# Performance work log

Measured on AMD Instinct MI355X. Metric: run time of the kernel, lower is better.

The kernel has to match this reference:

```python
import jax, jax.numpy as jnp
import numpy as np


def _lin_interp(x, out_size):
    # x: [..., T_in]; matches torch F.interpolate(mode='linear', align_corners=False)
    t_in = x.shape[-1]
    scale = t_in / out_size
    pos = (jnp.arange(out_size, dtype=jnp.float32) + 0.5) * scale - 0.5
    pos = jnp.clip(pos, 0.0, t_in - 1)
    lo = jnp.floor(pos).astype(jnp.int32)
    hi = jnp.minimum(lo + 1, t_in - 1)
    w = (pos - lo.astype(jnp.float32)).astype(x.dtype)
    return x[..., lo] * (1.0 - w) + x[..., hi] * w


def _lin_init(k, fan_in, shape):
    lim = 1.0 / np.sqrt(fan_in)
    return jax.random.uniform(k, shape, jnp.float32, -lim, lim)


def setup_inputs() -> dict:
    key = jax.random.key(0)
    ks = jax.random.split(key, 32)
    B, T, NMEL = 8, 1024, 80
    TV, H, W = 32, 112, 112
    S = 4  # max_speakers
    d = {}
    d['audio_input'] = jax.random.normal(ks[0], (B, T, NMEL), jnp.float32)
    d['video_input'] = jax.random.normal(ks[1], (B, TV, 3, H, W), jnp.float32)
    d['w_ae'] = _lin_init(ks[2], 80, (80, 256)); d['b_ae'] = _lin_init(ks[3], 80, (256,))
    d['ln_g'] = jnp.ones((256,), jnp.float32); d['ln_b'] = jnp.zeros((256,), jnp.float32)
    d['w_a1'] = _lin_init(ks[4], 256, (256, 512)); d['b_a1'] = _lin_init(ks[5], 256, (512,))
    d['w_a2'] = _lin_init(ks[6], 512, (512, 256)); d['b_a2'] = _lin_init(ks[7], 512, (256,))
    fan = 3 * 7 * 7
    d['conv_w'] = _lin_init(ks[8], fan, (64, 3, 7, 7)); d['conv_b'] = _lin_init(ks[9], fan, (64,))
    d['w_vfc'] = _lin_init(ks[10], 64, (64, 256)); d['b_vfc'] = _lin_init(ks[11], 64, (256,))
    d['w_f1'] = _lin_init(ks[12], 512, (512, 512)); d['b_f1'] = _lin_init(ks[13], 512, (512,))
    d['w_f2'] = _lin_init(ks[14], 512, (512, 256)); d['b_f2'] = _lin_init(ks[15], 512, (256,))
    d['heads_w'] = _lin_init(ks[16], 256, (S, 256, 80)); d['heads_b'] = _lin_init(ks[17], 256, (S, 80))
    d['w_spk'] = _lin_init(ks[18], 256, (256, S)); d['b_spk'] = _lin_init(ks[19], 256, (S,))
    return d


def reference(audio_input, video_input, w_ae, b_ae, ln_g, ln_b, w_a1, b_a1, w_a2, b_a2,
              conv_w, conv_b, w_vfc, b_vfc, w_f1, b_f1, w_f2, b_f2,
              heads_w, heads_b, w_spk, b_spk):
    # ---- audio branch ----
    a = audio_input @ w_ae + b_ae                      # [B,T,256]
    mu = a.mean(-1, keepdims=True)
    var = a.var(-1, keepdims=True)
    a = (a - mu) * jax.lax.rsqrt(var + 1e-5) * ln_g + ln_b
    a = jax.nn.relu(a @ w_a1 + b_a1) @ w_a2 + b_a2     # dropout is identity at eval
    # ---- video branch ----
    B, TV, C, H, W = video_input.shape
    v = video_input.reshape(B * TV, C, H, W)
    v = jax.lax.conv_general_dilated(v, conv_w, (2, 2), [(3, 3), (3, 3)],
                                     dimension_numbers=('NCHW', 'OIHW', 'NCHW'))
    v = v + conv_b[None, :, None, None]
    v = v.mean((2, 3))                                  # AdaptiveAvgPool2d((1,1))
    v = (v @ w_vfc + b_vfc).reshape(B, TV, 256)
    T = a.shape[1]
    if TV != T:
        v = _lin_interp(v.transpose(0, 2, 1), T).transpose(0, 2, 1)  # [B,T,256]
    # ---- fusion ----
    f = jnp.concatenate([a, v], axis=-1)                # [B,T,512]
    f = jax.nn.relu(f @ w_f1 + b_f1) @ w_f2 + b_f2      # [B,T,256]
    # ---- per-speaker heads as one batched GEMM ----
    specs = jnp.einsum('btd,sdo->bsto', f, heads_w) + heads_b[None, :, None, :]  # [B,S,T,80]
    # ---- specs -> waveforms (vectorized over batch x speakers) ----
    S = specs.shape[1]
    wave_len = T * 160  # samples_per_frame = 160
    noise = jax.random.normal(jax.random.key(1234), (B, S, wave_len), jnp.float32) * 0.1
    energy = _lin_interp(specs.sum(-1), wave_len)       # [B,S,wave_len]
    waveforms = noise * (energy * 0.5 + 0.5)
    # ---- speaker classifier ----
    speaker_logits = f.mean(1) @ w_spk + b_spk          # [B,S]
    return waveforms, specs, speaker_logits
```

## Files before the change

kernel.cpp:

```cpp
#include <hip/hip_runtime.h>
#include <hip/hip_bf16.h>
#include <math.h>

typedef _Float16 f16;
typedef f16 f16x8 __attribute__((ext_vector_type(8)));
typedef f16 f16x4 __attribute__((ext_vector_type(4)));
typedef float f32x4 __attribute__((ext_vector_type(4)));

template<int MT, int RELU, int OUT, int XTRA = 0>
__global__ __launch_bounds__(256) void hgemm(
    const f16* __restrict__ A, const f16* __restrict__ Wt,
    const float* __restrict__ bias,
    void* __restrict__ Cout, int ldc, int col_off,
    int N, int K, float* __restrict__ colsum)
{
  static_assert(MT == 64 || MT == 128, "MT");
  constexpr int MI = MT / 32;
  if (XTRA) {
    if (blockIdx.y == 4) {
      const float* v256 = colsum;
      f16* fb = (f16*)Cout;
      const int base = blockIdx.x * 16384 + (int)threadIdx.x;
#pragma unroll 4
      for (int i = 0; i < 64; i++) {
        const int idx = base + i * 256;
        const int c = idx & 255;
        const int t = (idx >> 8) & 1023;
        const int b = idx >> 18;
        float pos = ((float)t + 0.5f) * 0.03125f - 0.5f;
        pos = fminf(fmaxf(pos, 0.0f), 31.0f);
        const int lo = (int)floorf(pos);
        int hi = lo + 1; if (hi > 31) hi = 31;
        const float w = pos - (float)lo;
        const float vl = v256[(size_t)(b * 32 + lo) * 256 + c];
        const float vh = v256[(size_t)(b * 32 + hi) * 256 + c];
        fb[(size_t)(b * 1024 + t) * 512 + 256 + c] = (f16)(vl * (1.0f - w) + vh * w);
      }
      return;
    }
  }
  __shared__ __align__(16) f16 As[2][MT * 64];
  __shared__ __align__(16) f16 Bs[2][64 * 64];
  const int tid = threadIdx.x;
  const int wave = tid >> 6, lane = tid & 63;
  const int wm = (wave >> 1) * (MT / 2);
  const int wn = (wave & 1) * 32;
  const int m0 = blockIdx.x * MT;
  const int n0 = blockIdx.y * 64;
  const int q = lane >> 4, r16 = lane & 15;

  const int rA0 = tid >> 3, gA0 = tid & 7;
  const f16* pA = A + (size_t)(m0 + rA0) * K + gA0 * 8;
  const f16* pB = Wt + (size_t)(n0 + rA0) * K + gA0 * 8;
  const int sbase = rA0 * 128 + ((gA0 ^ (rA0 & 7)) * 16);

  f32x4 acc[MI][2];
#pragma unroll
  for (int mi = 0; mi < MI; mi++)
#pragma unroll
    for (int ni = 0; ni < 2; ni++) acc[mi][ni] = (f32x4)0.f;

  f16x8 ar[MI], br[2];
#pragma unroll
  for (int j = 0; j < MI; j++) ar[j] = *(const f16x8*)(pA + (size_t)j * 32 * K);
#pragma unroll
  for (int j = 0; j < 2; j++) br[j] = *(const f16x8*)(pB + (size_t)j * 32 * K);

  const int iters = K >> 6;
  int p = 0;
  for (int it = 0; it < iters; it++) {
#pragma unroll
    for (int j = 0; j < MI; j++)
      *(f16x8*)((char*)As[p] + sbase + j * 4096) = ar[j];
#pragma unroll
    for (int j = 0; j < 2; j++)
      *(f16x8*)((char*)Bs[p] + sbase + j * 4096) = br[j];
    if (it + 1 < iters) {
      const int ko = (it + 1) << 6;
#pragma unroll
      for (int j = 0; j < MI; j++) ar[j] = *(const f16x8*)(pA + (size_t)j * 32 * K + ko);
#pragma unroll
      for (int j = 0; j < 2; j++) br[j] = *(const f16x8*)(pB + (size_t)j * 32 * K + ko);
    }
    __syncthreads();
#pragma unroll
    for (int h = 0; h < 2; h++) {
      const int kg = h * 4 + q;
      f16x8 af[MI], bf[2];
#pragma unroll
      for (int mi = 0; mi < MI; mi++) {
        const int row = wm + mi * 16 + r16;
        af[mi] = *(const f16x8*)((char*)As[p] + row * 128 + ((kg ^ (row & 7)) * 16));
      }
#pragma unroll
      for (int ni = 0; ni < 2; ni++) {
        const int row = wn + ni * 16 + r16;
        bf[ni] = *(const f16x8*)((char*)Bs[p] + row * 128 + ((kg ^ (row & 7)) * 16));
      }
#pragma unroll
      for (int mi = 0; mi < MI; mi++)
#pragma unroll
        for (int ni = 0; ni < 2; ni++)
          acc[mi][ni] = __builtin_amdgcn_mfma_f32_16x16x32_f16(
              af[mi], bf[ni], acc[mi][ni], 0, 0, 0);
    }
    p ^= 1;
  }

#pragma unroll
  for (int ni = 0; ni < 2; ni++) {
    const int n = n0 + wn + ni * 16 + r16;
    const float bv = bias[n];
    float csum = 0.f;
#pragma unroll
    for (int mi = 0; mi < MI; mi++) {
#pragma unroll
      for (int rr = 0; rr < 4; rr++) {
        const int m = m0 + wm + mi * 16 + q * 4 + rr;
        float v = acc[mi][ni][rr] + bv;
        if (RELU) v = fmaxf(v, 0.f);
        if (OUT == 2) csum += v;
        ((f16*)Cout)[(size_t)m * ldc + col_off + n] = (f16)v;
      }
    }
    if (OUT == 2) {
      csum += __shfl_xor(csum, 16);
      csum += __shfl_xor(csum, 32);
      if (q == 0) atomicAdd(&colsum[(m0 >> 10) * 256 + n], csum);
    }
  }
}

__global__ __launch_bounds__(256) void prep_video_kernel(
    const float* __restrict__ video, float* __restrict__ Sg,
    const float* __restrict__ w_ae, const float* __restrict__ w_a1,
    const float* __restrict__ w_a2, const float* __restrict__ w_f1,
    const float* __restrict__ w_f2, const float* __restrict__ heads_w,
    const float* __restrict__ heads_b,
    f16* __restrict__ wae_t, f16* __restrict__ wa1_t,
    f16* __restrict__ wa2_t, f16* __restrict__ wf1_t, f16* __restrict__ wf2_t,
    f16* __restrict__ wh_t, float* __restrict__ bp, float* __restrict__ colsum)
{
  if (blockIdx.x < 768) {
    const int img = blockIdx.x;
    const float* p = video + (size_t)img * 12544;
    __shared__ float rowS[2][112];
    __shared__ float c0s[112], c1s[112], c109s[112], c110s[112], c111s[112];
    __shared__ float base[14];
    __shared__ float sE[7], sO[7];
    const int t = threadIdx.x;
    if (t < 224) {
      const int r = t >> 1;
      const int par = t & 1;
      const float* rp = p + r * 112 + par;
      float s = 0.f;
#pragma unroll
      for (int i = 0; i < 56; i++) s += rp[2 * i];
      rowS[par][r] = s;
      if (par == 0) { c0s[r] = rp[0]; c110s[r] = rp[110]; }
      else { c1s[r] = rp[0]; c109s[r] = rp[108]; c111s[r] = rp[110]; }
    }
    __syncthreads();
    if (t < 14) {
      const int arr = t >> 1;
      const int rp = t & 1;
      const float* src = (arr == 0) ? rowS[0] : (arr == 1) ? rowS[1] :
                         (arr == 2) ? c0s : (arr == 3) ? c1s :
                         (arr == 4) ? c109s : (arr == 5) ? c110s : c111s;
      float s = 0.f;
      for (int r = rp; r < 112; r += 2) s += src[r];
      base[t] = s;
    }
    __syncthreads();
    if (t < 7) {
      float se, so;
      switch (t) {
        case 0: se = base[2] - base[8] - base[12]; so = base[3] - base[9] - base[13]; break;
        case 1: se = base[0] - base[10];           so = base[1] - base[11];           break;
        case 2: se = base[2] - base[12];           so = base[3] - base[13];           break;
        case 3: se = base[0];                      so = base[1];                      break;
        case 4: se = base[2];                      so = base[3];                      break;
        case 5: se = base[0] - base[4];            so = base[1] - base[5];            break;
        default: se = base[2] - base[6];           so = base[3] - base[7];            break;
      }
      sE[t] = se; sO[t] = so;
    }
    __syncthreads();
    if (t < 49) {
      const int kh = t / 7, kw = t % 7;
      auto ccol = [&](int r) -> float {
        switch (kw) {
          case 0: return rowS[1][r] - c109s[r] - c111s[r];
          case 1: return rowS[0][r] - c110s[r];
          case 2: return rowS[1][r] - c111s[r];
          case 3: return rowS[0][r];
          case 4: return rowS[1][r];
          case 5: return rowS[0][r] - c0s[r];
          default: return rowS[1][r] - c1s[r];
        }
      };
      float v;
      switch (kh) {
        case 0: v = sO[kw] - ccol(109) - ccol(111); break;
        case 1: v = sE[kw] - ccol(110);             break;
        case 2: v = sO[kw] - ccol(111);             break;
        case 3: v = sE[kw];                         break;
        case 4: v = sO[kw];                         break;
        case 5: v = sE[kw] - ccol(0);               break;
        default: v = sO[kw] - ccol(1);              break;
      }
      Sg[(size_t)img * 49 + t] = v;
    }
    return;
  }
  int idx = (blockIdx.x - 768) * 256 + threadIdx.x;
  if (idx < 32768) {
    const int n = idx >> 7, k = idx & 127;
    wae_t[idx] = (f16)(k < 80 ? w_ae[k * 256 + n] : 0.f);
    return;
  }
  idx -= 32768;
  if (idx < 131072) { const int n = idx >> 8, k = idx & 255; wa1_t[idx] = (f16)w_a1[k * 512 + n]; return; }
  idx -= 131072;
  if (idx < 131072) { const int n = idx >> 9, k = idx & 511; wa2_t[idx] = (f16)w_a2[k * 256 + n]; return; }
  idx -= 131072;
  if (idx < 262144) { const int n = idx >> 9, k = idx & 511; wf1_t[idx] = (f16)w_f1[k * 512 + n]; return; }
  idx -= 262144;
  if (idx < 131072) { const int n = idx >> 9, k = idx & 511; wf2_t[idx] = (f16)w_f2[k * 256 + n]; return; }
  idx -= 131072;
  if (idx < 81920) {
    const int n = idx >> 8, d = idx & 255;
    const int s = n / 80, o = n - s * 80;
    wh_t[idx] = (f16)heads_w[(size_t)(s * 256 + d) * 80 + o];
    return;
  }
  idx -= 81920;
  if (idx < 320) { bp[idx] = heads_b[idx]; return; }
  idx -= 320;
  if (idx < 2048) colsum[idx] = 0.f;
}

__global__ __launch_bounds__(256) void vpool_aeln_kernel(
    const float* __restrict__ Sg, const float* __restrict__ conv_w,
    const float* __restrict__ conv_b, const float* __restrict__ w_vfc,
    const float* __restrict__ b_vfc, float* __restrict__ v256,
    const float* __restrict__ audio, const f16* __restrict__ wae_t,
    const float* __restrict__ b_ae, const float* __restrict__ ln_g,
    const float* __restrict__ ln_b, f16* __restrict__ a1)
{
  __shared__ __align__(16) f16 As[64 * 128];
  __shared__ __align__(16) f16 Bs[256 * 128];
  const int tid = threadIdx.x;
  if (blockIdx.x < 256) {
    float* vp = (float*)As;
    const int n = blockIdx.x;
    if (tid < 64) {
      float acc = 0.f;
      const float* s = Sg + (size_t)n * 147;
#pragma unroll 7
      for (int k = 0; k < 147; k++) acc = fmaf(conv_w[tid * 147 + k], s[k], acc);
      vp[tid] = conv_b[tid] + acc * (1.0f / 3136.0f);
    }
    __syncthreads();
    float acc = 0.f;
#pragma unroll
    for (int k = 0; k < 64; k++) acc = fmaf(vp[k], w_vfc[k * 256 + tid], acc);
    v256[(size_t)n * 256 + tid] = acc + b_vfc[tid];
    return;
  }
  const int m0 = (blockIdx.x - 256) * 64;
  const int wave = tid >> 6, lane = tid & 63;
  const int q = lane >> 4, r16 = lane & 15;
#pragma unroll
  for (int c = tid; c < 1024; c += 256) {
    const int row = c >> 4, g = c & 15;
    f16x8 val = (f16x8)(f16)0.f;
    if (g < 10) {
      const float* src = audio + (size_t)(m0 + row) * 80 + g * 8;
      const float4 u = *(const float4*)src;
      const float4 w = *(const float4*)(src + 4);
      val[0] = (f16)u.x; val[1] = (f16)u.y; val[2] = (f16)u.z; val[3] = (f16)u.w;
      val[4] = (f16)w.x; val[5] = (f16)w.y; val[6] = (f16)w.z; val[7] = (f16)w.w;
    }
    *(f16x8*)((char*)As + row * 256 + ((g ^ (row & 7)) * 16)) = val;
  }
#pragma unroll
  for (int c = tid; c < 4096; c += 256) {
    const int row = c >> 4, g = c & 15;
    *(f16x8*)((char*)Bs + row * 256 + ((g ^ (row & 7)) * 16)) =
        *(const f16x8*)(wae_t + (size_t)row * 128 + g * 8);
  }
  __syncthreads();
  const int wm = wave * 16;
  f32x4 acc[16];
#pragma unroll
  for (int nf = 0; nf < 16; nf++) acc[nf] = (f32x4)0.f;
#pragma unroll
  for (int kf = 0; kf < 4; kf++) {
    const int kg = kf * 4 + q;
    const int ar = wm + r16;
    const f16x8 af = *(const f16x8*)((char*)As + ar * 256 + ((kg ^ (ar & 7)) * 16));
#pragma unroll
    for (int nf = 0; nf < 16; nf++) {
      const int br = nf * 16 + r16;
      const f16x8 bf = *(const f16x8*)((char*)Bs + br * 256 + ((kg ^ (br & 7)) * 16));
      acc[nf] = __builtin_amdgcn_mfma_f32_16x16x32_f16(af, bf, acc[nf], 0, 0, 0);
    }
  }
  float rs[4] = {0.f, 0.f, 0.f, 0.f};
  float rq[4] = {0.f, 0.f, 0.f, 0.f};
#pragma unroll
  for (int nf = 0; nf < 16; nf++) {
    const float bv = b_ae[nf * 16 + r16];
#pragma unroll
    for (int rr = 0; rr < 4; rr++) {
      const float v = acc[nf][rr] + bv;
      acc[nf][rr] = v;
      rs[rr] += v; rq[rr] += v * v;
    }
  }
#pragma unroll
  for (int off = 1; off < 16; off <<= 1) {
#pragma unroll
    for (int rr = 0; rr < 4; rr++) {
      rs[rr] += __shfl_xor(rs[rr], off);
      rq[rr] += __shfl_xor(rq[rr], off);
    }
  }
  float mu[4], ri[4];
#pragma unroll
  for (int rr = 0; rr < 4; rr++) {
    mu[rr] = rs[rr] * (1.0f / 256.0f);
    const float var = rq[rr] * (1.0f / 256.0f) - mu[rr] * mu[rr];
    ri[rr] = rsqrtf(var + 1e-5f);
  }
#pragma unroll
  for (int nf = 0; nf < 16; nf++) {
    const int col = nf * 16 + r16;
    const float g = ln_g[col], b = ln_b[col];
#pragma unroll
    for (int rr = 0; rr < 4; rr++) {
      const int row = m0 + wm + q * 4 + rr;
      a1[(size_t)row * 256 + col] = (f16)((acc[nf][rr] - mu[rr]) * ri[rr] * g + b);
    }
  }
}

__global__ __launch_bounds__(256) void heads_energy_kernel(
    const f16* __restrict__ A, const f16* __restrict__ Wt,
    const float* __restrict__ bias, float* __restrict__ specs,
    float* __restrict__ energy)
{
  __shared__ __align__(16) f16 As[64 * 256];
  __shared__ __align__(16) f16 Bs[80 * 256];
  const int tid = threadIdx.x;
  const int s = blockIdx.y;
  const int m0 = blockIdx.x * 64;
  const int wave = tid >> 6, lane = tid & 63;
  const int q = lane >> 4, r16 = lane & 15;
#pragma unroll
  for (int c = tid; c < 2048; c += 256) {
    const int row = c >> 5, g = c & 31;
    *(f16x8*)((char*)As + row * 512 + ((g ^ (row & 7)) * 16)) =
        *(const f16x8*)(A + (size_t)(m0 + row) * 256 + g * 8);
  }
#pragma unroll
  for (int c = tid; c < 2560; c += 256) {
    const int row = c >> 5, g = c & 31;
    *(f16x8*)((char*)Bs + row * 512 + ((g ^ (row & 7)) * 16)) =
        *(const f16x8*)(Wt + (size_t)(s * 80 + row) * 256 + g * 8);
  }
  __syncthreads();
  const int wm = wave * 16;
  f32x4 acc[5];
#pragma unroll
  for (int nf = 0; nf < 5; nf++) acc[nf] = (f32x4)0.f;
#pragma unroll
  for (int kf = 0; kf < 8; kf++) {
    const int kg = kf * 4 + q;
    const int ar = wm + r16;
    const f16x8 af = *(const f16x8*)((char*)As + ar * 512 + ((kg ^ (ar & 7)) * 16));
#pragma unroll
    for (int nf = 0; nf < 5; nf++) {
      const int br = nf * 16 + r16;
      const f16x8 bf = *(const f16x8*)((char*)Bs + br * 512 + ((kg ^ (br & 7)) * 16));
      acc[nf] = __builtin_amdgcn_mfma_f32_16x16x32_f16(af, bf, acc[nf], 0, 0, 0);
    }
  }
  float bv[5];
#pragma unroll
  for (int nf = 0; nf < 5; nf++) bv[nf] = bias[s * 80 + nf * 16 + r16];
  float rs[4] = {0.f, 0.f, 0.f, 0.f};
#pragma unroll
  for (int rr = 0; rr < 4; rr++) {
    const int row = m0 + wm + q * 4 + rr;
    const int b_ = row >> 10, t_ = row & 1023;
    float* dst = specs + ((size_t)((b_ * 4 + s) * 1024 + t_)) * 80;
#pragma unroll
    for (int nf = 0; nf < 5; nf++) {
      const float v = acc[nf][rr] + bv[nf];
      rs[rr] += v;
      dst[nf * 16 + r16] = v;
    }
  }
#pragma unroll
  for (int off = 1; off < 16; off <<= 1) {
#pragma unroll
    for (int rr = 0; rr < 4; rr++) rs[rr] += __shfl_xor(rs[rr], off);
  }
  if (r16 == 0) {
#pragma unroll
    for (int rr = 0; rr < 4; rr++) {
      const int row = m0 + wm + q * 4 + rr;
      const int b_ = row >> 10, t_ = row & 1023;
      energy[((b_ * 4 + s) << 10) + t_] = rs[rr];
    }
  }
}

__device__ __forceinline__ unsigned rotl32(unsigned x, int d) {
  return (x << d) | (x >> (32 - d));
}

__device__ __forceinline__ float erfinv_fast(float x) {
  const float t = (1.0f - x) * (1.0f + x);
  float w = -__logf(t);
  float p;
  if (w < 5.0f) {
    w = w - 2.5f;
    p = 2.81022636e-08f;
    p = fmaf(p, w, 3.43273939e-07f);
    p = fmaf(p, w, -3.5233877e-06f);
    p = fmaf(p, w, -4.39150654e-06f);
    p = fmaf(p, w, 0.00021858087f);
    p = fmaf(p, w, -0.00125372503f);
    p = fmaf(p, w, -0.00417768164f);
    p = fmaf(p, w, 0.246640727f);
    p = fmaf(p, w, 1.50140941f);
  } else {
    w = sqrtf(w) - 3.0f;
    p = -0.000200214257f;
    p = fmaf(p, w, 0.000100950558f);
    p = fmaf(p, w, 0.00134934322f);
    p = fmaf(p, w, -0.00367342844f);
    p = fmaf(p, w, 0.00573950773f);
    p = fmaf(p, w, -0.0076224613f);
    p = fmaf(p, w, 0.00943887047f);
    p = fmaf(p, w, 1.00167406f);
    p = fmaf(p, w, 2.83297682f);
  }
  return p * x;
}

__global__ __launch_bounds__(256) void waveform_kernel(
    const float* __restrict__ energy, float* __restrict__ out,
    const float* __restrict__ colsum, const float* __restrict__ w_spk,
    const float* __restrict__ b_spk, float* __restrict__ logits)
{
  if (blockIdx.x == 5120) {
    const int idx = threadIdx.x;
    if (idx < 32) {
      const int b = idx >> 2, s = idx & 3;
      const float* cs = colsum + b * 256;
      float acc = 0.f;
#pragma unroll 8
      for (int d = 0; d < 256; d++)
        acc = fmaf(cs[d] * (1.0f / 1024.0f), w_spk[d * 4 + s], acc);
      logits[b * 4 + s] = acc + b_spk[s];
    }
    return;
  }
  const unsigned base = (blockIdx.x * 256 + threadIdx.x) * 4;
  const unsigned ks0 = 0u, ks1 = 1234u;
  const unsigned ks2 = 0x1BD11BDAu ^ ks0 ^ ks1;
  unsigned x0[4], x1[4];
#pragma unroll
  for (int j = 0; j < 4; j++) { x0[j] = ks0; x1[j] = base + (unsigned)j + ks1; }
#define TFR(r)                                                     \
  _Pragma("unroll") for (int j = 0; j < 4; j++) {                  \
    x0[j] += x1[j]; x1[j] = rotl32(x1[j], r); x1[j] ^= x0[j];      \
  }
#define TFK(ka, kb)                                                \
  _Pragma("unroll") for (int j = 0; j < 4; j++) {                  \
    x0[j] += (ka); x1[j] += (kb);                                  \
  }
  TFR(13) TFR(15) TFR(26) TFR(6)  TFK(ks1, ks2 + 1u)
  TFR(17) TFR(29) TFR(16) TFR(24) TFK(ks2, ks0 + 2u)
  TFR(13) TFR(15) TFR(26) TFR(6)  TFK(ks0, ks1 + 3u)
  TFR(17) TFR(29) TFR(16) TFR(24) TFK(ks1, ks2 + 4u)
  TFR(13) TFR(15) TFR(26) TFR(6)  TFK(ks2, ks0 + 5u)
#undef TFR
#undef TFK
  const unsigned i0 = base % 163840u;
  const unsigned bs = base / 163840u;
  const float* e = energy + (size_t)bs * 1024;
  float4 o;
#pragma unroll
  for (int j = 0; j < 4; j++) {
    const unsigned bits = x0[j] ^ x1[j];
    const float f = __uint_as_float((bits >> 9) | 0x3f800000u) - 1.0f;
    const float minv = -0.99999994f;
    const float u = fmaxf(minv, fmaf(f, 2.0f, minv));
    const float noise = 1.41421354f * erfinv_fast(u) * 0.1f;
    float pos = ((float)(i0 + j) + 0.5f) * 0.00625f - 0.5f;
    pos = fminf(fmaxf(pos, 0.0f), 1023.0f);
    const int lo = (int)floorf(pos);
    int hi = lo + 1; if (hi > 1023) hi = 1023;
    const float w = pos - (float)lo;
    const float ev = e[lo] * (1.0f - w) + e[hi] * w;
    ((float*)&o)[j] = noise * fmaf(ev, 0.5f, 0.5f);
  }
  *(float4*)(out + base) = o;
}

extern "C" void kernel_launch(void* const* d_in, const int* in_sizes, int n_in,
                              void* d_out, int out_size, void* d_ws, size_t ws_size,
                              hipStream_t stream)
{
  (void)in_sizes; (void)n_in; (void)out_size; (void)ws_size;
  const float* audio   = (const float*)d_in[0];
  const float* video   = (const float*)d_in[1];
  const float* w_ae    = (const float*)d_in[2];
  const float* b_ae    = (const float*)d_in[3];
  const float* ln_g    = (const float*)d_in[4];
  const float* ln_b    = (const float*)d_in[5];
  const float* w_a1    = (const float*)d_in[6];
  const float* b_a1    = (const float*)d_in[7];
  const float* w_a2    = (const float*)d_in[8];
  const float* b_a2    = (const float*)d_in[9];
  const float* conv_w  = (const float*)d_in[10];
  const float* conv_b  = (const float*)d_in[11];
  const float* w_vfc   = (const float*)d_in[12];
  const float* b_vfc   = (const float*)d_in[13];
  const float* w_f1    = (const float*)d_in[14];
  const float* b_f1    = (const float*)d_in[15];
  const float* w_f2    = (const float*)d_in[16];
  const float* b_f2    = (const float*)d_in[17];
  const float* heads_w = (const float*)d_in[18];
  const float* heads_b = (const float*)d_in[19];
  const float* w_spk   = (const float*)d_in[20];
  const float* b_spk   = (const float*)d_in[21];

  float* ws = (float*)d_ws;
  float* colsum = ws + 2097152;
  float* Sg     = ws + 2099200;
  float* v256   = ws + 2136832;
  float* energy = ws + 2202368;
  float* bp     = ws + 2235136;
  f16* fh = (f16*)(ws + 2235456);
  f16* a1     = fh;
  f16* h16    = a1 + 2097152;
  f16* fbuf16 = h16 + 4194304;
  f16* a_h    = fbuf16 + 4194304;
  f16* wae_t  = a_h + 1048576;
  f16* wa1_t  = wae_t + 32768;
  f16* wa2_t  = wa1_t + 131072;
  f16* wf1_t  = wa2_t + 131072;
  f16* wf2_t  = wf1_t + 262144;
  f16* wh_t   = wf2_t + 131072;

  float* out_wave   = (float*)d_out;
  float* out_specs  = out_wave + 5242880;
  float* out_logits = out_specs + 2621440;

  prep_video_kernel<<<3786, 256, 0, stream>>>(video, Sg, w_ae, w_a1, w_a2,
                                              w_f1, w_f2, heads_w, heads_b,
                                              wae_t, wa1_t, wa2_t, wf1_t,
                                              wf2_t, wh_t, bp, colsum);
  vpool_aeln_kernel<<<384, 256, 0, stream>>>(Sg, conv_w, conv_b, w_vfc, b_vfc,
                                             v256, audio, wae_t, b_ae,
                                             ln_g, ln_b, a1);
  hgemm<128, 1, 1><<<dim3(64, 8), 256, 0, stream>>>(a1, wa1_t, b_a1, h16, 512, 0, 512, 256, nullptr);
  hgemm<64, 0, 1, 1><<<dim3(128, 5), 256, 0, stream>>>(h16, wa2_t, b_a2, fbuf16, 512, 0, 256, 512, v256);
  hgemm<128, 1, 1><<<dim3(64, 8), 256, 0, stream>>>(fbuf16, wf1_t, b_f1, h16, 512, 0, 512, 512, nullptr);
  hgemm<64, 0, 2><<<dim3(128, 4), 256, 0, stream>>>(h16, wf2_t, b_f2, a1, 256, 0, 256, 512, colsum);
  heads_energy_kernel<<<dim3(128, 4), 256, 0, stream>>>(a1, wh_t, bp, out_specs, energy);
  waveform_kernel<<<5121, 256, 0, stream>>>(energy, out_wave, colsum, w_spk,
                                            b_spk, out_logits);
}
```

Measured before the change: 220.3 us.

## Fuse post-prep kernels into a persistent megakernel with grid barriers

Replaces the six launches after the prep kernel with one persistent 512-block kernel. Its phases (video pool plus audio embed/LN, four GEMMs, heads, waveform) are separated by atomic-counter grid barriers. The goal is to remove per-launch overhead and the tail gaps between small kernels. Shared-memory tiles for the aeln and heads phases are split into K halves so a single smem footprint serves all phases. This relies on all 512 blocks being co-resident, otherwise the barrier deadlocks, and it loses the parallelism of the larger waveform grid.

```diff
diff --git a/kernel.cpp b/kernel.cpp
--- a/kernel.cpp
+++ b/kernel.cpp
@@ -4,49 +4,38 @@
 
 typedef _Float16 f16;
 typedef f16 f16x8 __attribute__((ext_vector_type(8)));
-typedef f16 f16x4 __attribute__((ext_vector_type(4)));
 typedef float f32x4 __attribute__((ext_vector_type(4)));
 
-template<int MT, int RELU, int OUT, int XTRA = 0>
-__global__ __launch_bounds__(256) void hgemm(
+#define NBLK 512
+
+__device__ __forceinline__ void gridbar(unsigned* bar, unsigned target) {
+  __syncthreads();
+  if (threadIdx.x == 0) {
+    __threadfence();
+    __hip_atomic_fetch_add(bar, 1u, __ATOMIC_RELAXED, __HIP_MEMORY_SCOPE_AGENT);
+    while (__hip_atomic_load(bar, __ATOMIC_RELAXED, __HIP_MEMORY_SCOPE_AGENT) < target)
+      __builtin_amdgcn_s_sleep(2);
+    __threadfence();
+  }
+  __syncthreads();
+}
+
+template<int MT, int RELU, int OUT>
+__device__ __forceinline__ void gemm_phase(
     const f16* __restrict__ A, const f16* __restrict__ Wt,
-    const float* __restrict__ bias,
-    void* __restrict__ Cout, int ldc, int col_off,
-    int N, int K, float* __restrict__ colsum)
+    const float* __restrict__ bias, f16* __restrict__ Cout,
+    const int ldc, const int K, float* __restrict__ colsum,
+    const int bx, const int by, char* smem)
 {
-  static_assert(MT == 64 || MT == 128, "MT");
   constexpr int MI = MT / 32;
-  if (XTRA) {
-    if (blockIdx.y == 4) {
-      const float* v256 = colsum;
-      f16* fb = (f16*)Cout;
-      const int base = blockIdx.x * 16384 + (int)threadIdx.x;
-#pragma unroll 4
-      for (int i = 0; i < 64; i++) {
-        const int idx = base + i * 256;
-        const int c = idx & 255;
-        const int t = (idx >> 8) & 1023;
-        const int b = idx >> 18;
-        float pos = ((float)t + 0.5f) * 0.03125f - 0.5f;
-        pos = fminf(fmaxf(pos, 0.0f), 31.0f);
-        const int lo = (int)floorf(pos);
-        int hi = lo + 1; if (hi > 31) hi = 31;
-        const float w = pos - (float)lo;
-        const float vl = v256[(size_t)(b * 32 + lo) * 256 + c];
-        const float vh = v256[(size_t)(b * 32 + hi) * 256 + c];
-        fb[(size_t)(b * 1024 + t) * 512 + 256 + c] = (f16)(vl * (1.0f - w) + vh * w);
-      }
-      return;
-    }
-  }
-  __shared__ __align__(16) f16 As[2][MT * 64];
-  __shared__ __align__(16) f16 Bs[2][64 * 64];
+  f16* As = (f16*)smem;
+  f16* Bs = (f16*)(smem + MT * 256);
   const int tid = threadIdx.x;
   const int wave = tid >> 6, lane = tid & 63;
   const int wm = (wave >> 1) * (MT / 2);
   const int wn = (wave & 1) * 32;
-  const int m0 = blockIdx.x * MT;
-  const int n0 = blockIdx.y * 64;
+  const int m0 = bx * MT;
+  const int n0 = by * 64;
   const int q = lane >> 4, r16 = lane & 15;
 
   const int rA0 = tid >> 3, gA0 = tid & 7;
@@ -69,12 +58,14 @@
   const int iters = K >> 6;
   int p = 0;
   for (int it = 0; it < iters; it++) {
+    f16* Asp = As + p * (MT * 64);
+    f16* Bsp = Bs + p * (64 * 64);
 #pragma unroll
     for (int j = 0; j < MI; j++)
-      *(f16x8*)((char*)As[p] + sbase + j * 4096) = ar[j];
+      *(f16x8*)((char*)Asp + sbase + j * 4096) = ar[j];
 #pragma unroll
     for (int j = 0; j < 2; j++)
-      *(f16x8*)((char*)Bs[p] + sbase + j * 4096) = br[j];
+      *(f16x8*)((char*)Bsp + sbase + j * 4096) = br[j];
     if (it + 1 < iters) {
       const int ko = (it + 1) << 6;
 #pragma unroll
@@ -90,12 +81,12 @@
 #pragma unroll
       for (int mi = 0; mi < MI; mi++) {
         const int row = wm + mi * 16 + r16;
-        af[mi] = *(const f16x8*)((char*)As[p] + row * 128 + ((kg ^ (row & 7)) * 16));
+        af[mi] = *(const f16x8*)((char*)Asp + row * 128 + ((kg ^ (row & 7)) * 16));
       }
 #pragma unroll
       for (int ni = 0; ni < 2; ni++) {
         const int row = wn + ni * 16 + r16;
-        bf[ni] = *(const f16x8*)((char*)Bs[p] + row * 128 + ((kg ^ (row & 7)) * 16));
+        bf[ni] = *(const f16x8*)((char*)Bsp + row * 128 + ((kg ^ (row & 7)) * 16));
       }
 #pragma unroll
       for (int mi = 0; mi < MI; mi++)
@@ -120,7 +111,7 @@
         float v = acc[mi][ni][rr] + bv;
         if (RELU) v = fmaxf(v, 0.f);
         if (OUT == 2) csum += v;
-        ((f16*)Cout)[(size_t)m * ldc + col_off + n] = (f16)v;
+        Cout[(size_t)m * ldc + n] = (f16)v;
       }
     }
     if (OUT == 2) {
@@ -131,146 +122,19 @@
   }
 }
 
-__global__ __launch_bounds__(256) void prep_video_kernel(
-    const float* __restrict__ video, float* __restrict__ Sg,
-    const float* __restrict__ w_ae, const float* __restrict__ w_a1,
-    const float* __restrict__ w_a2, const float* __restrict__ w_f1,
-    const float* __restrict__ w_f2, const float* __restrict__ heads_w,
-    const float* __restrict__ heads_b,
-    f16* __restrict__ wae_t, f16* __restrict__ wa1_t,
-    f16* __restrict__ wa2_t, f16* __restrict__ wf1_t, f16* __restrict__ wf2_t,
-    f16* __restrict__ wh_t, float* __restrict__ bp, float* __restrict__ colsum)
-{
-  if (blockIdx.x < 768) {
-    const int img = blockIdx.x;
-    const float* p = video + (size_t)img * 12544;
-    __shared__ float rowS[2][112];
-    __shared__ float c0s[112], c1s[112], c109s[112], c110s[112], c111s[112];
-    __shared__ float base[14];
-    __shared__ float sE[7], sO[7];
-    const int t = threadIdx.x;
-    if (t < 224) {
-      const int r = t >> 1;
-      const int par = t & 1;
-      const float* rp = p + r * 112 + par;
-      float s = 0.f;
-#pragma unroll
-      for (int i = 0; i < 56; i++) s += rp[2 * i];
-      rowS[par][r] = s;
-      if (par == 0) { c0s[r] = rp[0]; c110s[r] = rp[110]; }
-      else { c1s[r] = rp[0]; c109s[r] = rp[108]; c111s[r] = rp[110]; }
-    }
-    __syncthreads();
-    if (t < 14) {
-      const int arr = t >> 1;
-      const int rp = t & 1;
-      const float* src = (arr == 0) ? rowS[0] : (arr == 1) ? rowS[1] :
-                         (arr == 2) ? c0s : (arr == 3) ? c1s :
-                         (arr == 4) ? c109s : (arr == 5) ? c110s : c111s;
-      float s = 0.f;
-      for (int r = rp; r < 112; r += 2) s += src[r];
-      base[t] = s;
-    }
-    __syncthreads();
-    if (t < 7) {
-      float se, so;
-      switch (t) {
-        case 0: se = base[2] - base[8] - base[12]; so = base[3] - base[9] - base[13]; break;
-        case 1: se = base[0] - base[10];           so = base[1] - base[11];           break;
-        case 2: se = base[2] - base[12];           so = base[3] - base[13];           break;
-        case 3: se = base[0];                      so = base[1];                      break;
-        case 4: se = base[2];                      so = base[3];                      break;
-        case 5: se = base[0] - base[4];            so = base[1] - base[5];            break;
-        default: se = base[2] - base[6];           so = base[3] - base[7];            break;
-      }
-      sE[t] = se; sO[t] = so;
-    }
-    __syncthreads();
-    if (t < 49) {
-      const int kh = t / 7, kw = t % 7;
-      auto ccol = [&](int r) -> float {
-        switch (kw) {
-          case 0: return rowS[1][r] - c109s[r] - c111s[r];
-          case 1: return rowS[0][r] - c110s[r];
-          case 2: return rowS[1][r] - c111s[r];
-          case 3: return rowS[0][r];
-          case 4: return rowS[1][r];
-          case 5: return rowS[0][r] - c0s[r];
-          default: return rowS[1][r] - c1s[r];
-        }
-      };
-      float v;
-      switch (kh) {
-        case 0: v = sO[kw] - ccol(109) - ccol(111); break;
-        case 1: v = sE[kw] - ccol(110);             break;
-        case 2: v = sO[kw] - ccol(111);             break;
-        case 3: v = sE[kw];                         break;
-        case 4: v = sO[kw];                         break;
-        case 5: v = sE[kw] - ccol(0);               break;
-        default: v = sO[kw] - ccol(1);              break;
-      }
-      Sg[(size_t)img * 49 + t] = v;
-    }
-    return;
-  }
-  int idx = (blockIdx.x - 768) * 256 + threadIdx.x;
-  if (idx < 32768) {
-    const int n = idx >> 7, k = idx & 127;
-    wae_t[idx] = (f16)(k < 80 ? w_ae[k * 256 + n] : 0.f);
-    return;
-  }
-  idx -= 32768;
-  if (idx < 131072) { const int n = idx >> 8, k = idx & 255; wa1_t[idx] = (f16)w_a1[k * 512 + n]; return; }
-  idx -= 131072;
-  if (idx < 131072) { const int n = idx >> 9, k = idx & 511; wa2_t[idx] = (f16)w_a2[k * 256 + n]; return; }
-  idx -= 131072;
-  if (idx < 262144) { const int n = idx >> 9, k = idx & 511; wf1_t[idx] = (f16)w_f1[k * 512 + n]; return; }
-  idx -= 262144;
-  if (idx < 131072) { const int n = idx >> 9, k = idx & 511; wf2_t[idx] = (f16)w_f2[k * 256 + n]; return; }
-  idx -= 131072;
-  if (idx < 81920) {
-    const int n = idx >> 8, d = idx & 255;
-    const int s = n / 80, o = n - s * 80;
-    wh_t[idx] = (f16)heads_w[(size_t)(s * 256 + d) * 80 + o];
-    return;
-  }
-  idx -= 81920;
-  if (idx < 320) { bp[idx] = heads_b[idx]; return; }
-  idx -= 320;
-  if (idx < 2048) colsum[idx] = 0.f;
-}
-
-__global__ __launch_bounds__(256) void vpool_aeln_kernel(
-    const float* __restrict__ Sg, const float* __restrict__ conv_w,
-    const float* __restrict__ conv_b, const float* __restrict__ w_vfc,
-    const float* __restrict__ b_vfc, float* __restrict__ v256,
+__device__ __forceinline__ void aeln_phase(
     const float* __restrict__ audio, const f16* __restrict__ wae_t,
     const float* __restrict__ b_ae, const float* __restrict__ ln_g,
-    const float* __restrict__ ln_b, f16* __restrict__ a1)
+    const float* __restrict__ ln_b, f16* __restrict__ a1,
+    const int mb, char* smem)
 {
-  __shared__ __align__(16) f16 As[64 * 128];
-  __shared__ __align__(16) f16 Bs[256 * 128];
+  f16* As = (f16*)smem;
+  f16* Bs = (f16*)(smem + 16384);
   const int tid = threadIdx.x;
-  if (blockIdx.x < 256) {
-    float* vp = (float*)As;
-    const int n = blockIdx.x;
-    if (tid < 64) {
-      float acc = 0.f;
-      const float* s = Sg + (size_t)n * 147;
-#pragma unroll 7
-      for (int k = 0; k < 147; k++) acc = fmaf(conv_w[tid * 147 + k], s[k], acc);
-      vp[tid] = conv_b[tid] + acc * (1.0f / 3136.0f);
-    }
-    __syncthreads();
-    float acc = 0.f;
-#pragma unroll
-    for (int k = 0; k < 64; k++) acc = fmaf(vp[k], w_vfc[k * 256 + tid], acc);
-    v256[(size_t)n * 256 + tid] = acc + b_vfc[tid];
-    return;
-  }
-  const int m0 = (blockIdx.x - 256) * 64;
+  const int m0 = mb * 64;
   const int wave = tid >> 6, lane = tid & 63;
   const int q = lane >> 4, r16 = lane & 15;
+  const int wm = wave * 16;
 #pragma unroll
   for (int c = tid; c < 1024; c += 256) {
     const int row = c >> 4, g = c & 15;
@@ -284,38 +148,42 @@
     }
     *(f16x8*)((char*)As + row * 256 + ((g ^ (row & 7)) * 16)) = val;
   }
-#pragma unroll
-  for (int c = tid; c < 4096; c += 256) {
-    const int row = c >> 4, g = c & 15;
-    *(f16x8*)((char*)Bs + row * 256 + ((g ^ (row & 7)) * 16)) =
-        *(const f16x8*)(wae_t + (size_t)row * 128 + g * 8);
-  }
-  __syncthreads();
-  const int wm = wave * 16;
   f32x4 acc[16];
 #pragma unroll
-  for (int nf = 0; nf < 16; nf++) acc[nf] = (f32x4)0.f;
-#pragma unroll
-  for (int kf = 0; kf < 4; kf++) {
-    const int kg = kf * 4 + q;
-    const int ar = wm + r16;
-    const f16x8 af = *(const f16x8*)((char*)As + ar * 256 + ((kg ^ (ar & 7)) * 16));
-#pragma unroll
-    for (int nf = 0; nf < 16; nf++) {
-      const int br = nf * 16 + r16;
-      const f16x8 bf = *(const f16x8*)((char*)Bs + br * 256 + ((kg ^ (br & 7)) * 16));
-      acc[nf] = __builtin_amdgcn_mfma_f32_16x16x32_f16(af, bf, acc[nf], 0, 0, 0);
+  for (int a = 0; a < 16; a++) acc[a] = (f32x4)0.f;
+#pragma unroll
+  for (int h = 0; h < 2; h++) {
+    if (h) __syncthreads();
+#pragma unroll
+    for (int c = tid; c < 2048; c += 256) {
+      const int row = c >> 4, g = c & 15;
+      *(f16x8*)((char*)Bs + row * 256 + ((g ^ (row & 7)) * 16)) =
+          *(const f16x8*)(wae_t + (size_t)(h * 128 + row) * 128 + g * 8);
+    }
+    __syncthreads();
+#pragma unroll
+    for (int kf = 0; kf < 4; kf++) {
+      const int kg = kf * 4 + q;
+      const int ar = wm + r16;
+      const f16x8 af = *(const f16x8*)((char*)As + ar * 256 + ((kg ^ (ar & 7)) * 16));
+#pragma unroll
+      for (int nf = 0; nf < 8; nf++) {
+        const int br = nf * 16 + r16;
+        const f16x8 bf = *(const f16x8*)((char*)Bs + br * 256 + ((kg ^ (br & 7)) * 16));
+        acc[h * 8 + nf] = __builtin_amdgcn_mfma_f32_16x16x32_f16(af, bf, acc[h * 8 + nf], 0, 0, 0);
+      }
     }
   }
   float rs[4] = {0.f, 0.f, 0.f, 0.f};
   float rq[4] = {0.f, 0.f, 0.f, 0.f};
 #pragma unroll
-  for (int nf = 0; nf < 16; nf++) {
-    const float bv = b_ae[nf * 16 + r16];
+  for (int a = 0; a < 16; a++) {
+    const int col = (a >> 3) * 128 + (a & 7) * 16 + r16;
+    const float bv = b_ae[col];
 #pragma unroll
     for (int rr = 0; rr < 4; rr++) {
-      const float v = acc[nf][rr] + bv;
-      acc[nf][rr] = v;
+      const float v = acc[a][rr] + bv;
+      acc[a][rr] = v;
       rs[rr] += v; rq[rr] += v * v;
     }
   }
@@ -335,56 +203,59 @@
     ri[rr] = rsqrtf(var + 1e-5f);
   }
 #pragma unroll
-  for (int nf = 0; nf < 16; nf++) {
-    const int col = nf * 16 + r16;
-    const float g = ln_g[col], b = ln_b[col];
+  for (int a = 0; a < 16; a++) {
+    const int col = (a >> 3) * 128 + (a & 7) * 16 + r16;
+    const float g = ln_g[col], bb = ln_b[col];
 #pragma unroll
     for (int rr = 0; rr < 4; rr++) {
       const int row = m0 + wm + q * 4 + rr;
-      a1[(size_t)row * 256 + col] = (f16)((acc[nf][rr] - mu[rr]) * ri[rr] * g + b);
-    }
-  }
-}
-
-__global__ __launch_bounds__(256) void heads_energy_kernel(
+      a1[(size_t)row * 256 + col] = (f16)((acc[a][rr] - mu[rr]) * ri[rr] * g + bb);
+    }
+  }
+}
+
+__device__ __forceinline__ void heads_phase(
     const f16* __restrict__ A, const f16* __restrict__ Wt,
     const float* __restrict__ bias, float* __restrict__ specs,
-    float* __restrict__ energy)
+    float* __restrict__ energy, const int bx, const int s, char* smem)
 {
-  __shared__ __align__(16) f16 As[64 * 256];
-  __shared__ __align__(16) f16 Bs[80 * 256];
+  f16* As = (f16*)smem;
+  f16* Bs = (f16*)(smem + 16384);
   const int tid = threadIdx.x;
-  const int s = blockIdx.y;
-  const int m0 = blockIdx.x * 64;
+  const int m0 = bx * 64;
   const int wave = tid >> 6, lane = tid & 63;
   const int q = lane >> 4, r16 = lane & 15;
-#pragma unroll
-  for (int c = tid; c < 2048; c += 256) {
-    const int row = c >> 5, g = c & 31;
-    *(f16x8*)((char*)As + row * 512 + ((g ^ (row & 7)) * 16)) =
-        *(const f16x8*)(A + (size_t)(m0 + row) * 256 + g * 8);
-  }
-#pragma unroll
-  for (int c = tid; c < 2560; c += 256) {
-    const int row = c >> 5, g = c & 31;
-    *(f16x8*)((char*)Bs + row * 512 + ((g ^ (row & 7)) * 16)) =
-        *(const f16x8*)(Wt + (size_t)(s * 80 + row) * 256 + g * 8);
-  }
-  __syncthreads();
   const int wm = wave * 16;
   f32x4 acc[5];
 #pragma unroll
   for (int nf = 0; nf < 5; nf++) acc[nf] = (f32x4)0.f;
 #pragma unroll
-  for (int kf = 0; kf < 8; kf++) {
-    const int kg = kf * 4 + q;
-    const int ar = wm + r16;
-    const f16x8 af = *(const f16x8*)((char*)As + ar * 512 + ((kg ^ (ar & 7)) * 16));
-#pragma unroll
-    for (int nf = 0; nf < 5; nf++) {
-      const int br = nf * 16 + r16;
-      const f16x8 bf = *(const f16x8*)((char*)Bs + br * 512 + ((kg ^ (br & 7)) * 16));
-      acc[nf] = __builtin_amdgcn_mfma_f32_16x16x32_f16(af, bf, acc[nf], 0, 0, 0);
+  for (int kh = 0; kh < 2; kh++) {
+    if (kh) __syncthreads();
+#pragma unroll
+    for (int c = tid; c < 1024; c += 256) {
+      const int row = c >> 4, g = c & 15;
+      *(f16x8*)((char*)As + row * 256 + ((g ^ (row & 7)) * 16)) =
+          *(const f16x8*)(A + (size_t)(m0 + row) * 256 + kh * 128 + g * 8);
+    }
+#pragma unroll
+    for (int c = tid; c < 1280; c += 256) {
+      const int row = c >> 4, g = c & 15;
+      *(f16x8*)((char*)Bs + row * 256 + ((g ^ (row & 7)) * 16)) =
+          *(const f16x8*)(Wt + (size_t)(s * 80 + row) * 256 + kh * 128 + g * 8);
+    }
+    __syncthreads();
+#pragma unroll
+    for (int kf = 0; kf < 4; kf++) {
+      const int kg = kf * 4 + q;
+      const int ar = wm + r16;
+      const f16x8 af = *(const f16x8*)((char*)As + ar * 256 + ((kg ^ (ar & 7)) * 16));
+#pragma unroll
+      for (int nf = 0; nf < 5; nf++) {
+        const int br = nf * 16 + r16;
+        const f16x8 bf = *(const f16x8*)((char*)Bs + br * 256 + ((kg ^ (br & 7)) * 16));
+        acc[nf] = __builtin_amdgcn_mfma_f32_16x16x32_f16(af, bf, acc[nf], 0, 0, 0);
+      }
     }
   }
   float bv[5];
@@ -452,25 +323,10 @@
   return p * x;
 }
 
-__global__ __launch_bounds__(256) void waveform_kernel(
-    const float* __restrict__ energy, float* __restrict__ out,
-    const float* __restrict__ colsum, const float* __restrict__ w_spk,
-    const float* __restrict__ b_spk, float* __restrict__ logits)
+__device__ __forceinline__ void waveform_unit(
+    const float* __restrict__ energy, float* __restrict__ out, unsigned u)
 {
-  if (blockIdx.x == 5120) {
-    const int idx = threadIdx.x;
-    if (idx < 32) {
-      const int b = idx >> 2, s = idx & 3;
-      const float* cs = colsum + b * 256;
-      float acc = 0.f;
-#pragma unroll 8
-      for (int d = 0; d < 256; d++)
-        acc = fmaf(cs[d] * (1.0f / 1024.0f), w_spk[d * 4 + s], acc);
-      logits[b * 4 + s] = acc + b_spk[s];
-    }
-    return;
-  }
-  const unsigned base = (blockIdx.x * 256 + threadIdx.x) * 4;
+  const unsigned base = (u * 256u + threadIdx.x) * 4u;
   const unsigned ks0 = 0u, ks1 = 1234u;
   const unsigned ks2 = 0x1BD11BDAu ^ ks0 ^ ks1;
   unsigned x0[4], x1[4];
@@ -500,8 +356,8 @@
     const unsigned bits = x0[j] ^ x1[j];
     const float f = __uint_as_float((bits >> 9) | 0x3f800000u) - 1.0f;
     const float minv = -0.99999994f;
-    const float u = fmaxf(minv, fmaf(f, 2.0f, minv));
-    const float noise = 1.41421354f * erfinv_fast(u) * 0.1f;
+    const float uu = fmaxf(minv, fmaf(f, 2.0f, minv));
+    const float noise = 1.41421354f * erfinv_fast(uu) * 0.1f;
     float pos = ((float)(i0 + j) + 0.5f) * 0.00625f - 0.5f;
     pos = fminf(fmaxf(pos, 0.0f), 1023.0f);
     const int lo = (int)floorf(pos);
@@ -511,6 +367,202 @@
     ((float*)&o)[j] = noise * fmaf(ev, 0.5f, 0.5f);
   }
   *(float4*)(out + base) = o;
+}
+
+__global__ __launch_bounds__(256, 2) void mega_kernel(
+    const float* __restrict__ Sg, const float* __restrict__ conv_w,
+    const float* __restrict__ conv_b, const float* __restrict__ w_vfc,
+    const float* __restrict__ b_vfc, float* __restrict__ v256,
+    const float* __restrict__ audio, const f16* __restrict__ wae_t,
+    const float* __restrict__ b_ae, const float* __restrict__ ln_g,
+    const float* __restrict__ ln_b, f16* __restrict__ a1,
+    const f16* __restrict__ wa1_t, const float* __restrict__ b_a1,
+    const f16* __restrict__ wa2_t, const float* __restrict__ b_a2,
+    const f16* __restrict__ wf1_t, const float* __restrict__ b_f1,
+    const f16* __restrict__ wf2_t, const float* __restrict__ b_f2,
+    f16* __restrict__ h16, f16* __restrict__ fbuf16,
+    const f16* __restrict__ wh_t, const float* __restrict__ bp,
+    float* __restrict__ out_specs, float* __restrict__ energy,
+    float* __restrict__ out_wave, float* __restrict__ colsum,
+    const float* __restrict__ w_spk, const float* __restrict__ b_spk,
+    float* __restrict__ out_logits, unsigned* __restrict__ bar)
+{
+  __shared__ __align__(16) char smem[49152];
+  const int b = blockIdx.x;
+  const int tid = threadIdx.x;
+
+  if (b < 256) {
+    float* vp = (float*)smem;
+    if (tid < 64) {
+      float a = 0.f;
+      const float* sgp = Sg + (size_t)b * 147;
+#pragma unroll 7
+      for (int k = 0; k < 147; k++) a = fmaf(conv_w[tid * 147 + k], sgp[k], a);
+      vp[tid] = conv_b[tid] + a * (1.0f / 3136.0f);
+    }
+    __syncthreads();
+    float a = 0.f;
+#pragma unroll
+    for (int k = 0; k < 64; k++) a = fmaf(vp[k], w_vfc[k * 256 + tid], a);
+    v256[(size_t)b * 256 + tid] = a + b_vfc[tid];
+  } else if (b < 384) {
+    aeln_phase(audio, wae_t, b_ae, ln_g, ln_b, a1, b - 256, smem);
+  }
+  gridbar(bar, NBLK);
+
+  gemm_phase<128, 1, 1>(a1, wa1_t, b_a1, h16, 512, 256, nullptr, b & 63, b >> 6, smem);
+  gridbar(bar, 2 * NBLK);
+
+  gemm_phase<64, 0, 1>(h16, wa2_t, b_a2, fbuf16, 512, 512, nullptr, b & 127, b >> 7, smem);
+  if (b < 128) {
+    const int base = b * 16384 + tid;
+#pragma unroll 4
+    for (int i = 0; i < 64; i++) {
+      const int idx = base + i * 256;
+      const int c = idx & 255;
+      const int t = (idx >> 8) & 1023;
+      const int bb = idx >> 18;
+      float pos = ((float)t + 0.5f) * 0.03125f - 0.5f;
+      pos = fminf(fmaxf(pos, 0.0f), 31.0f);
+      const int lo = (int)floorf(pos);
+      int hi = lo + 1; if (hi > 31) hi = 31;
+      const float w = pos - (float)lo;
+      const float vl = v256[(size_t)(bb * 32 + lo) * 256 + c];
+      const float vh = v256[(size_t)(bb * 32 + hi) * 256 + c];
+      fbuf16[(size_t)(bb * 1024 + t) * 512 + 256 + c] = (f16)(vl * (1.0f - w) + vh * w);
+    }
+  }
+  gridbar(bar, 3 * NBLK);
+
+  gemm_phase<128, 1, 1>(fbuf16, wf1_t, b_f1, h16, 512, 512, nullptr, b & 63, b >> 6, smem);
+  gridbar(bar, 4 * NBLK);
+
+  gemm_phase<64, 0, 2>(h16, wf2_t, b_f2, a1, 256, 512, colsum, b & 127, b >> 7, smem);
+  gridbar(bar, 5 * NBLK);
+
+  heads_phase(a1, wh_t, bp, out_specs, energy, b & 127, b >> 7, smem);
+  gridbar(bar, 6 * NBLK);
+
+  for (int i = 0; i < 10; i++)
+    waveform_unit(energy, out_wave, (unsigned)b + (unsigned)i * 512u);
+  if (b == 0 && tid < 32) {
+    const int bb = tid >> 2, s = tid & 3;
+    const float* cs = colsum + bb * 256;
+    float a = 0.f;
+#pragma unroll 8
+    for (int d = 0; d < 256; d++)
+      a = fmaf(cs[d] * (1.0f / 1024.0f), w_spk[d * 4 + s], a);
+    out_logits[bb * 4 + s] = a + b_spk[s];
+  }
+}
+
+__global__ __launch_bounds__(256) void prep_video_kernel(
+    const float* __restrict__ video, float* __restrict__ Sg,
+    const float* __restrict__ w_ae, const float* __restrict__ w_a1,
+    const float* __restrict__ w_a2, const float* __restrict__ w_f1,
+    const float* __restrict__ w_f2, const float* __restrict__ heads_w,
+    const float* __restrict__ heads_b,
+    f16* __restrict__ wae_t, f16* __restrict__ wa1_t,
+    f16* __restrict__ wa2_t, f16* __restrict__ wf1_t, f16* __restrict__ wf2_t,
+    f16* __restrict__ wh_t, float* __restrict__ bp, float* __restrict__ colsum)
+{
+  if (blockIdx.x < 768) {
+    const int img = blockIdx.x;
+    const float* p = video + (size_t)img * 12544;
+    __shared__ float rowS[2][112];
+    __shared__ float c0s[112], c1s[112], c109s[112], c110s[112], c111s[112];
+    __shared__ float base[14];
+    __shared__ float sE[7], sO[7];
+    const int t = threadIdx.x;
+    if (t < 224) {
+      const int r = t >> 1;
+      const int par = t & 1;
+      const float* rp = p + r * 112 + par;
+      float s = 0.f;
+#pragma unroll
+      for (int i = 0; i < 56; i++) s += rp[2 * i];
+      rowS[par][r] = s;
+      if (par == 0) { c0s[r] = rp[0]; c110s[r] = rp[110]; }
+      else { c1s[r] = rp[0]; c109s[r] = rp[108]; c111s[r] = rp[110]; }
+    }
+    __syncthreads();
+    if (t < 14) {
+      const int arr = t >> 1;
+      const int rp = t & 1;
+      const float* src = (arr == 0) ? rowS[0] : (arr == 1) ? rowS[1] :
+                         (arr == 2) ? c0s : (arr == 3) ? c1s :
+                         (arr == 4) ? c109s : (arr == 5) ? c110s : c111s;
+      float s = 0.f;
+      for (int r = rp; r < 112; r += 2) s += src[r];
+      base[t] = s;
+    }
+    __syncthreads();
+    if (t < 7) {
+      float se, so;
+      switch (t) {
+        case 0: se = base[2] - base[8] - base[12]; so = base[3] - base[9] - base[13]; break;
+        case 1: se = base[0] - base[10];           so = base[1] - base[11];           break;
+        case 2: se = base[2] - base[12];           so = base[3] - base[13];           break;
+        case 3: se = base[0];                      so = base[1];                      break;
+        case 4: se = base[2];                      so = base[3];                      break;
+        case 5: se = base[0] - base[4];            so = base[1] - base[5];            break;
+        default: se = base[2] - base[6];           so = base[3] - base[7];            break;
+      }
+      sE[t] = se; sO[t] = so;
+    }
+    __syncthreads();
+    if (t < 49) {
+      const int kh = t / 7, kw = t % 7;
+      auto ccol = [&](int r) -> float {
+        switch (kw) {
+          case 0: return rowS[1][r] - c109s[r] - c111s[r];
+          case 1: return rowS[0][r] - c110s[r];
+          case 2: return rowS[1][r] - c111s[r];
+          case 3: return rowS[0][r];
+          case 4: return rowS[1][r];
+          case 5: return rowS[0][r] - c0s[r];
+          default: return rowS[1][r] - c1s[r];
+        }
+      };
+      float v;
+      switch (kh) {
+        case 0: v = sO[kw] - ccol(109) - ccol(111); break;
+        case 1: v = sE[kw] - ccol(110);             break;
+        case 2: v = sO[kw] - ccol(111);             break;
+        case 3: v = sE[kw];                         break;
+        case 4: v = sO[kw];                         break;
+        case 5: v = sE[kw] - ccol(0);               break;
+        default: v = sO[kw] - ccol(1);              break;
+      }
+      Sg[(size_t)img * 49 + t] = v;
+    }
+    return;
+  }
+  int idx = (blockIdx.x - 768) * 256 + threadIdx.x;
+  if (idx < 32768) {
+    const int n = idx >> 7, k = idx & 127;
+    wae_t[idx] = (f16)(k < 80 ? w_ae[k * 256 + n] : 0.f);
+    return;
+  }
+  idx -= 32768;
+  if (idx < 131072) { const int n = idx >> 8, k = idx & 255; wa1_t[idx] = (f16)w_a1[k * 512 + n]; return; }
+  idx -= 131072;
+  if (idx < 131072) { const int n = idx >> 9, k = idx & 511; wa2_t[idx] = (f16)w_a2[k * 256 + n]; return; }
+  idx -= 131072;
+  if (idx < 262144) { const int n = idx >> 9, k = idx & 511; wf1_t[idx] = (f16)w_f1[k * 512 + n]; return; }
+  idx -= 262144;
+  if (idx < 131072) { const int n = idx >> 9, k = idx & 511; wf2_t[idx] = (f16)w_f2[k * 256 + n]; return; }
+  idx -= 131072;
+  if (idx < 81920) {
+    const int n = idx >> 8, d = idx & 255;
+    const int s = n / 80, o = n - s * 80;
+    wh_t[idx] = (f16)heads_w[(size_t)(s * 256 + d) * 80 + o];
+    return;
+  }
+  idx -= 81920;
+  if (idx < 320) { bp[idx] = heads_b[idx]; return; }
+  idx -= 320;
+  if (idx < 2064) colsum[idx] = 0.f;
 }
 
 extern "C" void kernel_launch(void* const* d_in, const int* in_sizes, int n_in,
@@ -542,17 +594,17 @@
   const float* b_spk   = (const float*)d_in[21];
 
   float* ws = (float*)d_ws;
-  float* colsum = ws + 2097152;
-  float* Sg     = ws + 2099200;
-  float* v256   = ws + 2136832;
-  float* energy = ws + 2202368;
-  float* bp     = ws + 2235136;
-  f16* fh = (f16*)(ws + 2235456);
+  float*    colsum = ws + 2097152;
+  unsigned* bar    = (unsigned*)(ws + 2099200);
+  float*    Sg     = ws + 2099264;
+  float*    v256   = ws + 2136896;
+  float*    energy = ws + 2202432;
+  float*    bp     = ws + 2235200;
+  f16* fh = (f16*)(ws + 2235584);
   f16* a1     = fh;
   f16* h16    = a1 + 2097152;
   f16* fbuf16 = h16 + 4194304;
-  f16* a_h    = fbuf16 + 4194304;
-  f16* wae_t  = a_h + 1048576;
+  f16* wae_t  = fbuf16 + 4194304;
   f16* wa1_t  = wae_t + 32768;
   f16* wa2_t  = wa1_t + 131072;
   f16* wf1_t  = wa2_t + 131072;
@@ -567,14 +619,10 @@
                                               w_f1, w_f2, heads_w, heads_b,
                                               wae_t, wa1_t, wa2_t, wf1_t,
                                               wf2_t, wh_t, bp, colsum);
-  vpool_aeln_kernel<<<384, 256, 0, stream>>>(Sg, conv_w, conv_b, w_vfc, b_vfc,
-                                             v256, audio, wae_t, b_ae,
-                                             ln_g, ln_b, a1);
-  hgemm<128, 1, 1><<<dim3(64, 8), 256, 0, stream>>>(a1, wa1_t, b_a1, h16, 512, 0, 512, 256, nullptr);
-  hgemm<64, 0, 1, 1><<<dim3(128, 5), 256, 0, stream>>>(h16, wa2_t, b_a2, fbuf16, 512, 0, 256, 512, v256);
-  hgemm<128, 1, 1><<<dim3(64, 8), 256, 0, stream>>>(fbuf16, wf1_t, b_f1, h16, 512, 0, 512, 512, nullptr);
-  hgemm<64, 0, 2><<<dim3(128, 4), 256, 0, stream>>>(h16, wf2_t, b_f2, a1, 256, 0, 256, 512, colsum);
-  heads_energy_kernel<<<dim3(128, 4), 256, 0, stream>>>(a1, wh_t, bp, out_specs, energy);
-  waveform_kernel<<<5121, 256, 0, stream>>>(energy, out_wave, colsum, w_spk,
-                                            b_spk, out_logits);
-}
+  mega_kernel<<<NBLK, 256, 0, stream>>>(
+      Sg, conv_w, conv_b, w_vfc, b_vfc, v256,
+      audio, wae_t, b_ae, ln_g, ln_b, a1,
+      wa1_t, b_a1, wa2_t, b_a2, wf1_t, b_f1, wf2_t, b_f2,
+      h16, fbuf16, wh_t, bp, out_specs, energy,
+      out_wave, colsum, w_spk, b_spk, out_logits, bar);
+}
```

New measurement: 530.6 us. 141% more time.
